# Optimization experiments

Hardware: AMD Instinct MI355X
Metric: run time of the kernel (lower is better)

Reference implementation:

```python
import jax, jax.numpy as jnp
import numpy as np

B, T, IN, OUT = 4, 8192, 512, 512
DIM, G, V, D = 32, 8, 8, 64  # quantizer dim, groups, num_vars, var_dim (vq_dim//groups)
TAU = 2.0  # initial gumbel temperature temp[0]
EPS = 1e-10


def setup_inputs() -> dict:
    key = jax.random.key(0)
    ks = jax.random.split(key, 8)
    s = lambda k, sh, f: (jax.random.normal(k, sh, jnp.float32) * f)
    return {
        "x": s(ks[0], (B, T, IN), 1.0),
        "W_pre": s(ks[1], (IN, DIM), IN ** -0.5),
        "b_pre": jnp.zeros((DIM,), jnp.float32),
        "W_proj": s(ks[2], (DIM, G * V), DIM ** -0.5),
        "b_proj": jnp.zeros((G * V,), jnp.float32),
        "codebook": s(ks[3], (G, V, D), 1.0),
        "W_post": s(ks[4], (G * D, OUT), (G * D) ** -0.5),
        "b_post": jnp.zeros((OUT,), jnp.float32),
        "u": jax.random.uniform(ks[5], (B, T, G, V), jnp.float32),
    }


def reference(x, W_pre, b_pre, W_proj, b_proj, codebook, W_post, b_post, u):
    b, t, _ = x.shape
    g, v, d = codebook.shape
    # pre-projection to quantizer dim, then logits over groups x num_vars
    h = x @ W_pre + b_pre                                # (B,T,32)
    logits = (h @ W_proj + b_proj).reshape(b, t, g, v)   # (B,T,G,V)
    # gumbel-softmax (hard, straight-through) as in F.gumbel_softmax
    gum = -jnp.log(-jnp.log(u + EPS) + EPS)
    y_soft = jax.nn.softmax((logits + gum) / TAU, axis=-1)
    hard = jax.nn.one_hot(jnp.argmax(y_soft, axis=-1), v, dtype=y_soft.dtype)
    w = hard + y_soft - jax.lax.stop_gradient(y_soft)    # (B,T,G,V)
    # codebook lookup: weighted sum over num_vars per group, concat groups
    q = jnp.einsum("btgv,gvd->btgd", w, codebook).reshape(b, t, g * d)
    return q @ W_post + b_post                           # (B,T,OUT)
```

## Files before the change

### kernel.cpp

```cpp
#include <hip/hip_runtime.h>
#include <hip/hip_bf16.h>
#include <stdint.h>
#include <stddef.h>

#define BT_TOK   32768
#define IN_DIM   512
#define OUT_DIM  512
#define QDIM     32
#define GV       64
#define NG       8
#define NV       8
#define VD       64
#define EPS_G    1e-10f

#define MT       64
#define BK       64
#define NTHR     256

__global__ __launch_bounds__(128) void build_p2(
    const float* __restrict__ codebook,
    const float* __restrict__ W_post,
    __hip_bfloat16* __restrict__ P2)
{
    const int b  = blockIdx.x;
    const int p  = b >> 6;
    const int ij = b & 63;
    const int i  = ij >> 3, j = ij & 7;
    const int t  = threadIdx.x;

    const float* ca = codebook + ((size_t)(2 * p) * NV + i) * VD;
    const float* cb = codebook + ((size_t)(2 * p + 1) * NV + j) * VD;
    const float* wa = W_post + (size_t)(2 * p) * VD * OUT_DIM;
    const float* wb = W_post + (size_t)(2 * p + 1) * VD * OUT_DIM;

    float acc[4] = {0.f, 0.f, 0.f, 0.f};
    for (int d = 0; d < VD; ++d) {
        const float a  = ca[d];
        const float bb = cb[d];
        const float* ra = wa + (size_t)d * OUT_DIM;
        const float* rb = wb + (size_t)d * OUT_DIM;
#pragma unroll
        for (int q = 0; q < 4; ++q) {
            const int o = t + q * 128;
            acc[q] += a * ra[o] + bb * rb[o];
        }
    }
    __hip_bfloat16* dst = P2 + ((size_t)(p * 64 + ij)) * OUT_DIM;
#pragma unroll
    for (int q = 0; q < 4; ++q)
        dst[t + q * 128] = __float2bfloat16(acc[q]);
}

__global__ __launch_bounds__(256) void fused_main(
    const float* __restrict__ x,
    const float* __restrict__ W_pre,
    const float* __restrict__ b_pre,
    const float* __restrict__ W_proj,
    const float* __restrict__ b_proj,
    const float* __restrict__ u,
    const float* __restrict__ b_post,
    const __hip_bfloat16* __restrict__ P2,
    float* __restrict__ out)
{
    __shared__ float Xs[MT][BK + 4];
    __shared__ float Ws[BK][QDIM];
    __shared__ float Wp[QDIM][GV];
    __shared__ float Hs[MT][QDIM + 4];
    __shared__ int   idxs[MT][NG];
    __shared__ int   pidxs[MT][4];

    const int t = threadIdx.x;
    const int tokbase = blockIdx.x * MT;

    {
        const float4* src = (const float4*)W_proj;
        float4* dst = (float4*)&Wp[0][0];
        dst[t]       = src[t];
        dst[t + 256] = src[t + 256];
    }

    const int n4 = (t & 7) * 4;
    const int tm = (t >> 3) * 2;
    const float4 bp = *(const float4*)&b_pre[n4];
    float acc0[4] = {bp.x, bp.y, bp.z, bp.w};
    float acc1[4] = {bp.x, bp.y, bp.z, bp.w};

    const int xrow = t >> 2;
    const int xq   = t & 3;

    for (int k0 = 0; k0 < IN_DIM; k0 += BK) {
        __syncthreads();
        {
            const float4* src =
                (const float4*)(x + (size_t)(tokbase + xrow) * IN_DIM + k0);
#pragma unroll
            for (int uq = 0; uq < 4; ++uq) {
                float4 v = src[xq + 4 * uq];
                *(float4*)&Xs[xrow][4 * (xq + 4 * uq)] = v;
            }
        }
        {
            const float4* src = (const float4*)(W_pre + (size_t)k0 * QDIM);
            float4* dst = (float4*)&Ws[0][0];
            dst[t]       = src[t];
            dst[t + 256] = src[t + 256];
        }
        __syncthreads();

#pragma unroll 16
        for (int kk = 0; kk < BK; ++kk) {
            const float a0 = Xs[tm][kk];
            const float a1 = Xs[tm + 1][kk];
            const float4 w = *(const float4*)&Ws[kk][n4];
            acc0[0] += a0 * w.x; acc0[1] += a0 * w.y;
            acc0[2] += a0 * w.z; acc0[3] += a0 * w.w;
            acc1[0] += a1 * w.x; acc1[1] += a1 * w.y;
            acc1[2] += a1 * w.z; acc1[3] += a1 * w.w;
        }
    }

    __syncthreads();
    *(float4*)&Hs[tm][n4]     = make_float4(acc0[0], acc0[1], acc0[2], acc0[3]);
    *(float4*)&Hs[tm + 1][n4] = make_float4(acc1[0], acc1[1], acc1[2], acc1[3]);
    __syncthreads();

#pragma unroll
    for (int tt = 0; tt < 2; ++tt) {
        const int task = t + tt * 256;
        const int tok  = task >> 3;
        const int g    = task & 7;

        const float4 bj0 = *(const float4*)&b_proj[g * 8];
        const float4 bj1 = *(const float4*)&b_proj[g * 8 + 4];
        float lg[8] = {bj0.x, bj0.y, bj0.z, bj0.w, bj1.x, bj1.y, bj1.z, bj1.w};

#pragma unroll
        for (int j = 0; j < QDIM; ++j) {
            const float hv = Hs[tok][j];
            const float4 w0 = *(const float4*)&Wp[j][g * 8];
            const float4 w1 = *(const float4*)&Wp[j][g * 8 + 4];
            lg[0] += hv * w0.x; lg[1] += hv * w0.y;
            lg[2] += hv * w0.z; lg[3] += hv * w0.w;
            lg[4] += hv * w1.x; lg[5] += hv * w1.y;
            lg[6] += hv * w1.z; lg[7] += hv * w1.w;
        }

        const float4* up = (const float4*)(u + (size_t)tokbase * GV);
        const float4 u0 = up[task * 2];
        const float4 u1 = up[task * 2 + 1];
        float y[8];
        y[0] = lg[0] - logf(-logf(u0.x + EPS_G) + EPS_G);
        y[1] = lg[1] - logf(-logf(u0.y + EPS_G) + EPS_G);
        y[2] = lg[2] - logf(-logf(u0.z + EPS_G) + EPS_G);
        y[3] = lg[3] - logf(-logf(u0.w + EPS_G) + EPS_G);
        y[4] = lg[4] - logf(-logf(u1.x + EPS_G) + EPS_G);
        y[5] = lg[5] - logf(-logf(u1.y + EPS_G) + EPS_G);
        y[6] = lg[6] - logf(-logf(u1.z + EPS_G) + EPS_G);
        y[7] = lg[7] - logf(-logf(u1.w + EPS_G) + EPS_G);

        float best = y[0];
        int bi = 0;
#pragma unroll
        for (int v = 1; v < 8; ++v) {
            if (y[v] > best) { best = y[v]; bi = v; }
        }
        idxs[tok][g] = bi;
    }
    __syncthreads();

    {
        const int tok = t >> 2, p = t & 3;
        pidxs[tok][p] = idxs[tok][2 * p] * 8 + idxs[tok][2 * p + 1];
    }
    __syncthreads();

    const int o2 = t * 2;
    const float b0 = b_post[o2];
    const float b1 = b_post[o2 + 1];
    float* outp = out + (size_t)tokbase * OUT_DIM;
    const uint16_t* p2u = (const uint16_t*)P2;

#pragma unroll 4
    for (int tok = 0; tok < MT; ++tok) {
        float r0 = b0, r1 = b1;
#pragma unroll
        for (int p = 0; p < 4; ++p) {
            const int pi = pidxs[tok][p];
            const uint32_t raw =
                *(const uint32_t*)(p2u + ((size_t)(p * 64 + pi) * OUT_DIM + o2));
            r0 += __uint_as_float(raw << 16);
            r1 += __uint_as_float(raw & 0xffff0000u);
        }
        *(float2*)&outp[(size_t)tok * OUT_DIM + o2] = make_float2(r0, r1);
    }
}

extern "C" void kernel_launch(void* const* d_in, const int* in_sizes, int n_in,
                              void* d_out, int out_size, void* d_ws, size_t ws_size,
                              hipStream_t stream) {
    const float* x        = (const float*)d_in[0];
    const float* W_pre    = (const float*)d_in[1];
    const float* b_pre    = (const float*)d_in[2];
    const float* W_proj   = (const float*)d_in[3];
    const float* b_proj   = (const float*)d_in[4];
    const float* codebook = (const float*)d_in[5];
    const float* W_post   = (const float*)d_in[6];
    const float* b_post   = (const float*)d_in[7];
    const float* u        = (const float*)d_in[8];
    float* out = (float*)d_out;

    __hip_bfloat16* P2 = (__hip_bfloat16*)d_ws;

    build_p2<<<256, 128, 0, stream>>>(codebook, W_post, P2);
    fused_main<<<BT_TOK / MT, NTHR, 0, stream>>>(x, W_pre, b_pre, W_proj, b_proj,
                                                 u, b_post, P2, out);
}
```

Before: 185.3 us.

## Restructure pre-projection to per-lane tokens with split-K across waves

Replaces the LDS-staged x/W_pre tiling with a scheme where each lane owns one token and each wave handles a quarter of the input dimension. Partial sums are reduced through shared memory. W_pre and W_proj are read directly with wave-uniform addresses, and each wave computes logits for two groups. This removes LDS staging and several barriers, at the cost of strided per-lane x loads and higher register pressure. build_p2 also switches to 256 threads.

```diff
diff --git a/kernel.cpp b/kernel.cpp
--- a/kernel.cpp
+++ b/kernel.cpp
@@ -7,17 +7,14 @@
 #define IN_DIM   512
 #define OUT_DIM  512
 #define QDIM     32
-#define GV       64
 #define NG       8
 #define NV       8
 #define VD       64
 #define EPS_G    1e-10f
 
 #define MT       64
-#define BK       64
-#define NTHR     256
-
-__global__ __launch_bounds__(128) void build_p2(
+
+__global__ __launch_bounds__(256) void build_p2(
     const float* __restrict__ codebook,
     const float* __restrict__ W_post,
     __hip_bfloat16* __restrict__ P2)
@@ -28,30 +25,25 @@
     const int i  = ij >> 3, j = ij & 7;
     const int t  = threadIdx.x;
 
-    const float* ca = codebook + ((size_t)(2 * p) * NV + i) * VD;
-    const float* cb = codebook + ((size_t)(2 * p + 1) * NV + j) * VD;
-    const float* wa = W_post + (size_t)(2 * p) * VD * OUT_DIM;
-    const float* wb = W_post + (size_t)(2 * p + 1) * VD * OUT_DIM;
-
-    float acc[4] = {0.f, 0.f, 0.f, 0.f};
+    const float* ca  = codebook + ((size_t)(2 * p) * NV + i) * VD;
+    const float* cbp = codebook + ((size_t)(2 * p + 1) * NV + j) * VD;
+    const float* wa  = W_post + (size_t)(2 * p) * VD * OUT_DIM;
+    const float* wb  = W_post + (size_t)(2 * p + 1) * VD * OUT_DIM;
+
+    float a0 = 0.f, a1 = 0.f;
+#pragma unroll 8
     for (int d = 0; d < VD; ++d) {
-        const float a  = ca[d];
-        const float bb = cb[d];
-        const float* ra = wa + (size_t)d * OUT_DIM;
-        const float* rb = wb + (size_t)d * OUT_DIM;
-#pragma unroll
-        for (int q = 0; q < 4; ++q) {
-            const int o = t + q * 128;
-            acc[q] += a * ra[o] + bb * rb[o];
-        }
+        const float sa = ca[d];
+        const float sb = cbp[d];
+        a0 += sa * wa[(size_t)d * OUT_DIM + t]       + sb * wb[(size_t)d * OUT_DIM + t];
+        a1 += sa * wa[(size_t)d * OUT_DIM + t + 256] + sb * wb[(size_t)d * OUT_DIM + t + 256];
     }
     __hip_bfloat16* dst = P2 + ((size_t)(p * 64 + ij)) * OUT_DIM;
-#pragma unroll
-    for (int q = 0; q < 4; ++q)
-        dst[t + q * 128] = __float2bfloat16(acc[q]);
+    dst[t]       = __float2bfloat16(a0);
+    dst[t + 256] = __float2bfloat16(a1);
 }
 
-__global__ __launch_bounds__(256) void fused_main(
+__global__ __launch_bounds__(256, 3) void fused_main(
     const float* __restrict__ x,
     const float* __restrict__ W_pre,
     const float* __restrict__ b_pre,
@@ -62,92 +54,88 @@
     const __hip_bfloat16* __restrict__ P2,
     float* __restrict__ out)
 {
-    __shared__ float Xs[MT][BK + 4];
-    __shared__ float Ws[BK][QDIM];
-    __shared__ float Wp[QDIM][GV];
-    __shared__ float Hs[MT][QDIM + 4];
-    __shared__ int   idxs[MT][NG];
-    __shared__ int   pidxs[MT][4];
-
-    const int t = threadIdx.x;
+    __shared__ float Hs4[4][MT][36];
+    __shared__ int   pidx_s[4][MT];
+
+    const int t    = threadIdx.x;
+    const int lane = t & 63;
+    const int w    = __builtin_amdgcn_readfirstlane(t >> 6);
     const int tokbase = blockIdx.x * MT;
-
-    {
-        const float4* src = (const float4*)W_proj;
-        float4* dst = (float4*)&Wp[0][0];
-        dst[t]       = src[t];
-        dst[t + 256] = src[t + 256];
-    }
-
-    const int n4 = (t & 7) * 4;
-    const int tm = (t >> 3) * 2;
-    const float4 bp = *(const float4*)&b_pre[n4];
-    float acc0[4] = {bp.x, bp.y, bp.z, bp.w};
-    float acc1[4] = {bp.x, bp.y, bp.z, bp.w};
-
-    const int xrow = t >> 2;
-    const int xq   = t & 3;
-
-    for (int k0 = 0; k0 < IN_DIM; k0 += BK) {
-        __syncthreads();
-        {
-            const float4* src =
-                (const float4*)(x + (size_t)(tokbase + xrow) * IN_DIM + k0);
-#pragma unroll
-            for (int uq = 0; uq < 4; ++uq) {
-                float4 v = src[xq + 4 * uq];
-                *(float4*)&Xs[xrow][4 * (xq + 4 * uq)] = v;
-            }
+    const int gtok    = tokbase + lane;
+
+    float acc[QDIM];
+#pragma unroll
+    for (int j = 0; j < QDIM; ++j) acc[j] = 0.f;
+
+    const float* xrow = x + (size_t)gtok * IN_DIM + w * 128;
+
+    for (int c = 0; c < 4; ++c) {
+        float4 xr[8];
+#pragma unroll
+        for (int f = 0; f < 8; ++f)
+            xr[f] = ((const float4*)xrow)[c * 8 + f];
+
+        const float* wbase = W_pre + (size_t)(w * 128 + c * 32) * QDIM;
+#pragma unroll
+        for (int kk = 0; kk < 32; ++kk) {
+            const float xv = ((const float*)xr)[kk];
+            const float4* wr = (const float4*)(wbase + (size_t)kk * QDIM);
+            const float4 w0 = wr[0], w1 = wr[1], w2 = wr[2], w3 = wr[3];
+            const float4 w4 = wr[4], w5 = wr[5], w6 = wr[6], w7 = wr[7];
+            acc[0]  += xv * w0.x; acc[1]  += xv * w0.y; acc[2]  += xv * w0.z; acc[3]  += xv * w0.w;
+            acc[4]  += xv * w1.x; acc[5]  += xv * w1.y; acc[6]  += xv * w1.z; acc[7]  += xv * w1.w;
+            acc[8]  += xv * w2.x; acc[9]  += xv * w2.y; acc[10] += xv * w2.z; acc[11] += xv * w2.w;
+            acc[12] += xv * w3.x; acc[13] += xv * w3.y; acc[14] += xv * w3.z; acc[15] += xv * w3.w;
+            acc[16] += xv * w4.x; acc[17] += xv * w4.y; acc[18] += xv * w4.z; acc[19] += xv * w4.w;
+            acc[20] += xv * w5.x; acc[21] += xv * w5.y; acc[22] += xv * w5.z; acc[23] += xv * w5.w;
+            acc[24] += xv * w6.x; acc[25] += xv * w6.y; acc[26] += xv * w6.z; acc[27] += xv * w6.w;
+            acc[28] += xv * w7.x; acc[29] += xv * w7.y; acc[30] += xv * w7.z; acc[31] += xv * w7.w;
         }
-        {
-            const float4* src = (const float4*)(W_pre + (size_t)k0 * QDIM);
-            float4* dst = (float4*)&Ws[0][0];
-            dst[t]       = src[t];
-            dst[t + 256] = src[t + 256];
+    }
+
+#pragma unroll
+    for (int j4 = 0; j4 < 8; ++j4)
+        *(float4*)&Hs4[w][lane][j4 * 4] =
+            make_float4(acc[j4 * 4], acc[j4 * 4 + 1], acc[j4 * 4 + 2], acc[j4 * 4 + 3]);
+    __syncthreads();
+
+#pragma unroll
+    for (int r = 0; r < 8; ++r) {
+        const int id  = t + 256 * r;
+        const int tok = id >> 5;
+        const int j   = id & 31;
+        const float h = b_pre[j] + Hs4[0][tok][j] + Hs4[1][tok][j]
+                                 + Hs4[2][tok][j] + Hs4[3][tok][j];
+        Hs4[0][tok][j] = h;
+    }
+    __syncthreads();
+
+    float h[QDIM];
+#pragma unroll
+    for (int j4 = 0; j4 < 8; ++j4) {
+        const float4 v = *(const float4*)&Hs4[0][lane][j4 * 4];
+        h[j4 * 4] = v.x; h[j4 * 4 + 1] = v.y; h[j4 * 4 + 2] = v.z; h[j4 * 4 + 3] = v.w;
+    }
+
+    int idx2[2];
+#pragma unroll
+    for (int gg = 0; gg < 2; ++gg) {
+        const int g = 2 * w + gg;
+        const float4 b0 = *(const float4*)&b_proj[g * 8];
+        const float4 b1 = *(const float4*)&b_proj[g * 8 + 4];
+        float lg[8] = {b0.x, b0.y, b0.z, b0.w, b1.x, b1.y, b1.z, b1.w};
+
+#pragma unroll
+        for (int j = 0; j < QDIM; ++j) {
+            const float hv = h[j];
+            const float4 a0 = *(const float4*)&W_proj[(size_t)j * 64 + g * 8];
+            const float4 a1 = *(const float4*)&W_proj[(size_t)j * 64 + g * 8 + 4];
+            lg[0] += hv * a0.x; lg[1] += hv * a0.y; lg[2] += hv * a0.z; lg[3] += hv * a0.w;
+            lg[4] += hv * a1.x; lg[5] += hv * a1.y; lg[6] += hv * a1.z; lg[7] += hv * a1.w;
         }
-        __syncthreads();
-
-#pragma unroll 16
-        for (int kk = 0; kk < BK; ++kk) {
-            const float a0 = Xs[tm][kk];
-            const float a1 = Xs[tm + 1][kk];
-            const float4 w = *(const float4*)&Ws[kk][n4];
-            acc0[0] += a0 * w.x; acc0[1] += a0 * w.y;
-            acc0[2] += a0 * w.z; acc0[3] += a0 * w.w;
-            acc1[0] += a1 * w.x; acc1[1] += a1 * w.y;
-            acc1[2] += a1 * w.z; acc1[3] += a1 * w.w;
-        }
-    }
-
-    __syncthreads();
-    *(float4*)&Hs[tm][n4]     = make_float4(acc0[0], acc0[1], acc0[2], acc0[3]);
-    *(float4*)&Hs[tm + 1][n4] = make_float4(acc1[0], acc1[1], acc1[2], acc1[3]);
-    __syncthreads();
-
-#pragma unroll
-    for (int tt = 0; tt < 2; ++tt) {
-        const int task = t + tt * 256;
-        const int tok  = task >> 3;
-        const int g    = task & 7;
-
-        const float4 bj0 = *(const float4*)&b_proj[g * 8];
-        const float4 bj1 = *(const float4*)&b_proj[g * 8 + 4];
-        float lg[8] = {bj0.x, bj0.y, bj0.z, bj0.w, bj1.x, bj1.y, bj1.z, bj1.w};
-
-#pragma unroll
-        for (int j = 0; j < QDIM; ++j) {
-            const float hv = Hs[tok][j];
-            const float4 w0 = *(const float4*)&Wp[j][g * 8];
-            const float4 w1 = *(const float4*)&Wp[j][g * 8 + 4];
-            lg[0] += hv * w0.x; lg[1] += hv * w0.y;
-            lg[2] += hv * w0.z; lg[3] += hv * w0.w;
-            lg[4] += hv * w1.x; lg[5] += hv * w1.y;
-            lg[6] += hv * w1.z; lg[7] += hv * w1.w;
-        }
-
-        const float4* up = (const float4*)(u + (size_t)tokbase * GV);
-        const float4 u0 = up[task * 2];
-        const float4 u1 = up[task * 2 + 1];
+
+        const float4 u0 = *(const float4*)&u[(size_t)gtok * 64 + g * 8];
+        const float4 u1 = *(const float4*)&u[(size_t)gtok * 64 + g * 8 + 4];
         float y[8];
         y[0] = lg[0] - logf(-logf(u0.x + EPS_G) + EPS_G);
         y[1] = lg[1] - logf(-logf(u0.y + EPS_G) + EPS_G);
@@ -161,37 +149,35 @@
         float best = y[0];
         int bi = 0;
 #pragma unroll
-        for (int v = 1; v < 8; ++v) {
+        for (int v = 1; v < 8; ++v)
             if (y[v] > best) { best = y[v]; bi = v; }
-        }
-        idxs[tok][g] = bi;
-    }
+        idx2[gg] = bi;
+    }
+    pidx_s[w][lane] = idx2[0] * 8 + idx2[1];
     __syncthreads();
 
-    {
-        const int tok = t >> 2, p = t & 3;
-        pidxs[tok][p] = idxs[tok][2 * p] * 8 + idxs[tok][2 * p + 1];
-    }
-    __syncthreads();
-
     const int o2 = t * 2;
-    const float b0 = b_post[o2];
-    const float b1 = b_post[o2 + 1];
-    float* outp = out + (size_t)tokbase * OUT_DIM;
-    const uint16_t* p2u = (const uint16_t*)P2;
+    const float bp0 = b_post[o2];
+    const float bp1 = b_post[o2 + 1];
+    float* orow = out + (size_t)tokbase * OUT_DIM;
+    const uint32_t* p2u = (const uint32_t*)P2;
 
 #pragma unroll 4
     for (int tok = 0; tok < MT; ++tok) {
-        float r0 = b0, r1 = b1;
-#pragma unroll
-        for (int p = 0; p < 4; ++p) {
-            const int pi = pidxs[tok][p];
-            const uint32_t raw =
-                *(const uint32_t*)(p2u + ((size_t)(p * 64 + pi) * OUT_DIM + o2));
-            r0 += __uint_as_float(raw << 16);
-            r1 += __uint_as_float(raw & 0xffff0000u);
-        }
-        *(float2*)&outp[(size_t)tok * OUT_DIM + o2] = make_float2(r0, r1);
+        const int p0 = pidx_s[0][tok];
+        const int p1 = pidx_s[1][tok];
+        const int p2i = pidx_s[2][tok];
+        const int p3 = pidx_s[3][tok];
+        const uint32_t r0 = p2u[(size_t)(0 * 64 + p0) * 256 + t];
+        const uint32_t r1 = p2u[(size_t)(1 * 64 + p1) * 256 + t];
+        const uint32_t r2 = p2u[(size_t)(2 * 64 + p2i) * 256 + t];
+        const uint32_t r3 = p2u[(size_t)(3 * 64 + p3) * 256 + t];
+        float s0 = bp0, s1 = bp1;
+        s0 += __uint_as_float(r0 << 16); s1 += __uint_as_float(r0 & 0xffff0000u);
+        s0 += __uint_as_float(r1 << 16); s1 += __uint_as_float(r1 & 0xffff0000u);
+        s0 += __uint_as_float(r2 << 16); s1 += __uint_as_float(r2 & 0xffff0000u);
+        s0 += __uint_as_float(r3 << 16); s1 += __uint_as_float(r3 & 0xffff0000u);
+        *(float2*)&orow[(size_t)tok * OUT_DIM + o2] = make_float2(s0, s1);
     }
 }
 
@@ -211,7 +197,7 @@
 
     __hip_bfloat16* P2 = (__hip_bfloat16*)d_ws;
 
-    build_p2<<<256, 128, 0, stream>>>(codebook, W_post, P2);
-    fused_main<<<BT_TOK / MT, NTHR, 0, stream>>>(x, W_pre, b_pre, W_proj, b_proj,
-                                                 u, b_post, P2, out);
+    build_p2<<<256, 256, 0, stream>>>(codebook, W_post, P2);
+    fused_main<<<BT_TOK / MT, 256, 0, stream>>>(x, W_pre, b_pre, W_proj, b_proj,
+                                                u, b_post, P2, out);
 }
```

After: 169.6 us. 8.5% less time.
